# Kernel tuning notes

Measured on AMD Instinct MI355X. Metric: run time of the kernel, lower is better.

Reference implementation:

```python
import jax, jax.numpy as jnp
import numpy as np

C = 64
CQ = C // 8
B, D, H, W = 4, 16, 16, 16


def setup_inputs() -> dict:
    key = jax.random.key(0)
    ks = jax.random.split(key, 8)
    s = 1.0 / np.sqrt(C)
    return {
        "x": jax.random.normal(ks[0], (B, C, D, H, W), jnp.float32),
        "Wq": jax.random.normal(ks[1], (CQ, C), jnp.float32) * s,
        "bq": jax.random.normal(ks[2], (CQ,), jnp.float32) * 0.01,
        "Wk": jax.random.normal(ks[3], (CQ, C), jnp.float32) * s,
        "bk": jax.random.normal(ks[4], (CQ,), jnp.float32) * 0.01,
        "Wv": jax.random.normal(ks[5], (C, C), jnp.float32) * s,
        "bv": jax.random.normal(ks[6], (C,), jnp.float32) * 0.01,
        "gamma": jnp.zeros((1,), jnp.float32) + 0.5,
    }


def reference(x, Wq, bq, Wk, bk, Wv, bv, gamma):
    b, c, d, h, w = x.shape
    n = d * h * w
    xf = x.reshape(b, c, n)  # [b, c, n]
    # 1x1x1 Conv3d == pointwise linear over channel dim
    q = jnp.einsum('oc,bcn->bon', Wq, xf) + bq[None, :, None]  # [b, cq, n]
    k = jnp.einsum('oc,bcn->bon', Wk, xf) + bk[None, :, None]  # [b, cq, n]
    v = jnp.einsum('oc,bcn->bon', Wv, xf) + bv[None, :, None]  # [b, c, n]
    # attn[b, i, j] = softmax_j(q[:, :, i] . k[:, :, j])
    scores = jnp.einsum('bci,bcj->bij', q, k)  # [b, n, n]
    attn = jax.nn.softmax(scores, axis=-1)
    # out = v @ attn^T : out[b, c, i] = sum_j v[b, c, j] * attn[b, i, j]
    out = jnp.einsum('bcj,bij->bci', v, attn).reshape(b, c, d, h, w)
    return gamma * out + x
```

## Files before the change

### kernel.cpp

```cpp
#include <hip/hip_runtime.h>
#include <hip/hip_bf16.h>
#include <cmath>

#define NTOK 4096

typedef float        f32x16 __attribute__((ext_vector_type(16)));
typedef short        s16x8  __attribute__((ext_vector_type(8)));
typedef unsigned int u32x4  __attribute__((ext_vector_type(4)));

__device__ __forceinline__ unsigned short f2bf(float f) {
    __hip_bfloat16 h = __float2bfloat16(f);
    return *reinterpret_cast<unsigned short*>(&h);
}
__device__ __forceinline__ float bf2f(unsigned short u) {
    __hip_bfloat16 h = *reinterpret_cast<__hip_bfloat16*>(&u);
    return __bfloat162float(h);
}
__device__ __forceinline__ unsigned pk2(float a, float b) {
    __hip_bfloat162 h = __float22bfloat162_rn(make_float2(a, b));
    return *reinterpret_cast<unsigned*>(&h);
}

__global__ __launch_bounds__(512)
void qkv_kernel(const float* __restrict__ x,
                const float* __restrict__ Wq, const float* __restrict__ bq,
                const float* __restrict__ Wk, const float* __restrict__ bk,
                const float* __restrict__ Wv, const float* __restrict__ bv,
                unsigned short* __restrict__ qt2, unsigned short* __restrict__ kt2,
                unsigned short* __restrict__ vt)
{
    __shared__ float wlds[80 * 64];
    __shared__ float blds[80];
    __shared__ float pacc[2][4][32][9];

    const int t  = threadIdx.x;
    const int l  = t & 63;
    const int wv = t >> 6;
    const int cq = wv & 3;
    const int cp = wv >> 2;
    const int v  = l & 31;
    const int hh = l >> 5;

    for (int idx = t; idx < 1280; idx += 512) {
        const int row  = idx >> 4;
        const int col4 = idx & 15;
        const float* src = (row < 8)  ? (Wq + row * 64)
                         : (row < 16) ? (Wk + (row - 8) * 64)
                                      : (Wv + (row - 16) * 64);
        ((float4*)wlds)[idx] = ((const float4*)src)[col4];
    }
    if (t < 80)
        blds[t] = (t < 8) ? bq[t] : (t < 16) ? bk[t - 8] : bv[t - 16];
    __syncthreads();

    const int vg = blockIdx.x;
    const int b  = vg >> 7;
    const int i  = ((vg & 127) << 5) + v;

    const float* xb = x + ((size_t)b * 64 + 16 * cq) * NTOK + i;
    float xv[16];
    #pragma unroll
    for (int c = 0; c < 16; c++) xv[c] = xb[(size_t)c * NTOK];

    const size_t row = (size_t)b * NTOK + i;
    const int jl   = i & 15;
    const int slot = (jl & 3) | ((jl & 4) << 1) | ((jl & 8) >> 1);

    #pragma unroll
    for (int s = 0; s < 5; ++s) {
        const int chunk = cp + 2 * s;

        float a[4];
        #pragma unroll
        for (int k = 0; k < 4; k++) a[k] = 0.f;
        #pragma unroll
        for (int c4 = 0; c4 < 4; c4++) {
            #pragma unroll
            for (int k = 0; k < 4; k++) {
                const float4 w4v =
                    ((const float4*)wlds)[(chunk * 8 + 4 * hh + k) * 16 + cq * 4 + c4];
                a[k] += w4v.x * xv[c4*4+0] + w4v.y * xv[c4*4+1]
                      + w4v.z * xv[c4*4+2] + w4v.w * xv[c4*4+3];
            }
        }
        if (s) __syncthreads();
        #pragma unroll
        for (int k = 0; k < 4; k++) pacc[cp][cq][v][4 * hh + k] = a[k];
        __syncthreads();

        const int o = 2 * cq + hh;
        float fin = ((pacc[cp][0][v][o] + pacc[cp][1][v][o])
                  +  (pacc[cp][2][v][o] + pacc[cp][3][v][o]))
                  + blds[chunk * 8 + o];

        if (chunk < 2) {
            if (chunk == 0) fin *= 1.4426950408889634f;
            const unsigned short hu = f2bf(fin);
            const unsigned short lu = f2bf(fin - bf2f(hu));
            unsigned short* dst = (chunk == 0 ? qt2 : kt2) + row * 16;
            dst[o]     = hu;
            dst[8 + o] = lu;
        } else {
            const int c = (chunk - 2) * 8 + o;
            vt[((size_t)b * 256 + (i >> 4)) * 1024 + (size_t)c * 16 + slot] = f2bf(fin);
        }
    }
}

__global__ __launch_bounds__(1024)
void attn_kernel(const unsigned short* __restrict__ qt2,
                 const unsigned short* __restrict__ kt2,
                 const unsigned short* __restrict__ vt,
                 const float* __restrict__ x,
                 const float* __restrict__ gamma,
                 float* __restrict__ out)
{
    __shared__ float slds[4][64][64];
    __shared__ float sldl[4][64];

    const int t    = threadIdx.x;
    const int l    = t & 63;
    const int wv   = t >> 6;
    const int qt   = wv & 1;
    const int u    = wv >> 1;
    const int lo31 = l & 31;
    const int h    = l >> 5;
    const int w     = blockIdx.x;
    const int b     = w >> 6;
    const int qbase = (w & 63) << 6;
    const int j0    = u << 9;

    const unsigned short* qrow =
        qt2 + ((size_t)b * NTOK + qbase + qt * 32 + lo31) * 16;
    s16x8 qB1 = *(const s16x8*)qrow;
    s16x8 qB2;
    if (h == 0) qB2 = *(const s16x8*)(qrow + 8);
    else        { u32x4 z = {0,0,0,0}; qB2 = __builtin_bit_cast(s16x8, z); }

    const unsigned short* kb  = kt2 + (size_t)b * NTOK * 16 + (size_t)h * 8;
    const unsigned short* vbA = vt + (size_t)b * NTOK * 64 + (size_t)lo31 * 16 + 8 * h;
    const unsigned short* vbB = vbA + 512;

    f32x16 accA, accB;
    #pragma unroll
    for (int r = 0; r < 16; r++) { accA[r] = 0.f; accB[r] = 0.f; }
    float lsum = 0.f;

    s16x8 K[2], V00[2], V01[2], V10[2], V11[2];

    #define LOADSET(s_, a_) do {                                              \
        K[s_]   = *(const s16x8*)(kb + (size_t)(j0 + ((a_) << 5) + lo31) * 16);  \
        V00[s_] = *(const s16x8*)(vbA + (size_t)((j0 >> 4) + ((a_) << 1)) * 1024);     \
        V01[s_] = *(const s16x8*)(vbA + (size_t)((j0 >> 4) + ((a_) << 1) + 1) * 1024); \
        V10[s_] = *(const s16x8*)(vbB + (size_t)((j0 >> 4) + ((a_) << 1)) * 1024);     \
        V11[s_] = *(const s16x8*)(vbB + (size_t)((j0 >> 4) + ((a_) << 1) + 1) * 1024); \
    } while (0)

    LOADSET(0, 0);

    #pragma unroll
    for (int it = 0; it < 16; ++it) {
        const int cu = it & 1;
        const int nx = it + 1;
        LOADSET(cu ^ 1, (nx < 16) ? nx : 0);

        f32x16 s;
        #pragma unroll
        for (int r = 0; r < 16; r++) s[r] = 0.f;
        s = __builtin_amdgcn_mfma_f32_32x32x16_bf16(K[cu], qB1, s, 0, 0, 0);
        s = __builtin_amdgcn_mfma_f32_32x32x16_bf16(K[cu], qB2, s, 0, 0, 0);

        #pragma unroll
        for (int r = 0; r < 16; r++) s[r] = __builtin_amdgcn_exp2f(s[r]);

        lsum += ((s[0]+s[1])+(s[2]+s[3])) + ((s[4]+s[5])+(s[6]+s[7]))
              + ((s[8]+s[9])+(s[10]+s[11])) + ((s[12]+s[13])+(s[14]+s[15]));

        u32x4 wa, wc;
        wa.x = pk2(s[0], s[1]);   wa.y = pk2(s[2], s[3]);
        wa.z = pk2(s[4], s[5]);   wa.w = pk2(s[6], s[7]);
        wc.x = pk2(s[8], s[9]);   wc.y = pk2(s[10], s[11]);
        wc.z = pk2(s[12], s[13]); wc.w = pk2(s[14], s[15]);
        s16x8 pf0 = __builtin_bit_cast(s16x8, wa);
        s16x8 pf1 = __builtin_bit_cast(s16x8, wc);

        __builtin_amdgcn_s_setprio(1);
        accA = __builtin_amdgcn_mfma_f32_32x32x16_bf16(V00[cu], pf0, accA, 0, 0, 0);
        accA = __builtin_amdgcn_mfma_f32_32x32x16_bf16(V01[cu], pf1, accA, 0, 0, 0);
        accB = __builtin_amdgcn_mfma_f32_32x32x16_bf16(V10[cu], pf0, accB, 0, 0, 0);
        accB = __builtin_amdgcn_mfma_f32_32x32x16_bf16(V11[cu], pf1, accB, 0, 0, 0);
        __builtin_amdgcn_s_setprio(0);
    }

    lsum += __shfl_xor(lsum, 32);

    #define WR_SLOT(sidx) do {                                                \
        const int s_ = (sidx);                                                \
        _Pragma("unroll")                                                     \
        for (int r = 0; r < 16; r++) {                                        \
            const int c_ = (r & 3) + 8 * (r >> 2) + 4 * h;                    \
            slds[s_][c_][qt * 32 + lo31]      = accA[r];                      \
            slds[s_][c_ + 32][qt * 32 + lo31] = accB[r];                      \
        }                                                                     \
        if (h == 0) sldl[s_][qt * 32 + lo31] = lsum;                          \
    } while (0)

    #define MRG_SLOT(sidx) do {                                               \
        const int s_ = (sidx);                                                \
        _Pragma("unroll")                                                     \
        for (int r = 0; r < 16; r++) {                                        \
            const int c_ = (r & 3) + 8 * (r >> 2) + 4 * h;                    \
            accA[r] += slds[s_][c_][qt * 32 + lo31];                          \
            accB[r] += slds[s_][c_ + 32][qt * 32 + lo31];                     \
        }                                                                     \
        lsum += sldl[s_][qt * 32 + lo31];                                     \
    } while (0)

    if (u >= 4) WR_SLOT(u - 4);
    __syncthreads();
    if (u < 4) MRG_SLOT(u);
    __syncthreads();
    if (u == 2 || u == 3) WR_SLOT(u - 2);
    __syncthreads();
    if (u < 2) MRG_SLOT(u);
    __syncthreads();
    if (u == 1) WR_SLOT(0);
    __syncthreads();
    if (u == 0) { MRG_SLOT(0); WR_SLOT(0); }
    __syncthreads();

    const int c  = t >> 4;
    const int q4 = (t & 15) << 2;
    const float g = gamma[0];
    const float4 a4 = *(const float4*)&slds[0][c][q4];
    const float g0 = g / sldl[0][q4 + 0];
    const float g1 = g / sldl[0][q4 + 1];
    const float g2 = g / sldl[0][q4 + 2];
    const float g3 = g / sldl[0][q4 + 3];
    const size_t off = (((size_t)b * 64 + c) << 12) + qbase + q4;
    const float4 xv4 = *(const float4*)(x + off);
    float4 o;
    o.x = a4.x * g0 + xv4.x;
    o.y = a4.y * g1 + xv4.y;
    o.z = a4.z * g2 + xv4.z;
    o.w = a4.w * g3 + xv4.w;
    *(float4*)(out + off) = o;
}

extern "C" void kernel_launch(void* const* d_in, const int* in_sizes, int n_in,
                              void* d_out, int out_size, void* d_ws, size_t ws_size,
                              hipStream_t stream) {
    const float* x     = (const float*)d_in[0];
    const float* Wq    = (const float*)d_in[1];
    const float* bq    = (const float*)d_in[2];
    const float* Wk    = (const float*)d_in[3];
    const float* bk    = (const float*)d_in[4];
    const float* Wv    = (const float*)d_in[5];
    const float* bv    = (const float*)d_in[6];
    const float* gamma = (const float*)d_in[7];
    float* out = (float*)d_out;

    unsigned short* qt2 = (unsigned short*)d_ws;
    unsigned short* kt2 = qt2 + (size_t)4 * NTOK * 16;
    unsigned short* vt  = kt2 + (size_t)4 * NTOK * 16;

    qkv_kernel<<<512, 512, 0, stream>>>(x, Wq, bq, Wk, bk, Wv, bv, qt2, kt2, vt);
    attn_kernel<<<256, 1024, 0, stream>>>(qt2, kt2, vt, x, gamma, out);
}
```

Measured before the change: 33.82 us.

## Compute QKV projection with bf16 MFMA instead of scalar FMA and LDS reduction

The QKV projection kernel is rewritten to use 32x32x16 bf16 MFMA instructions. Each wave now computes all 80 output rows for 32 tokens directly from global memory, so the LDS weight staging, the cross-wave partial-sum reduction and the barriers are gone. The launch shrinks from 512 blocks of 512 threads to 128 blocks of 256. This rounds x and the weights to bf16 before accumulation, where they were fp32 before, which may hurt accuracy, particularly for the q/k hi-lo split.

```diff
diff --git a/kernel.cpp b/kernel.cpp
--- a/kernel.cpp
+++ b/kernel.cpp
@@ -21,7 +21,7 @@
     return *reinterpret_cast<unsigned*>(&h);
 }
 
-__global__ __launch_bounds__(512)
+__global__ __launch_bounds__(256, 4)
 void qkv_kernel(const float* __restrict__ x,
                 const float* __restrict__ Wq, const float* __restrict__ bq,
                 const float* __restrict__ Wk, const float* __restrict__ bk,
@@ -29,80 +29,85 @@
                 unsigned short* __restrict__ qt2, unsigned short* __restrict__ kt2,
                 unsigned short* __restrict__ vt)
 {
-    __shared__ float wlds[80 * 64];
-    __shared__ float blds[80];
-    __shared__ float pacc[2][4][32][9];
-
-    const int t  = threadIdx.x;
-    const int l  = t & 63;
-    const int wv = t >> 6;
-    const int cq = wv & 3;
-    const int cp = wv >> 2;
-    const int v  = l & 31;
-    const int hh = l >> 5;
-
-    for (int idx = t; idx < 1280; idx += 512) {
-        const int row  = idx >> 4;
-        const int col4 = idx & 15;
-        const float* src = (row < 8)  ? (Wq + row * 64)
-                         : (row < 16) ? (Wk + (row - 8) * 64)
-                                      : (Wv + (row - 16) * 64);
-        ((float4*)wlds)[idx] = ((const float4*)src)[col4];
+    const int t    = threadIdx.x;
+    const int l    = t & 63;
+    const int wv   = t >> 6;
+    const int lo31 = l & 31;
+    const int h    = l >> 5;
+    const int blk  = blockIdx.x;
+    const int b    = blk >> 5;
+    const int i    = ((blk & 31) << 7) + (wv << 5) + lo31;
+
+    const float* xb = x + ((size_t)b * 64) * NTOK + i;
+    s16x8 B0, B1, B2, B3;
+    #define MAKE_B(Bv, ks) do {                                               \
+        const float* src = xb + (size_t)((ks) * 16 + 8 * h) * NTOK;           \
+        float f0 = src[0];                  float f1 = src[NTOK];             \
+        float f2 = src[2 * (size_t)NTOK];   float f3 = src[3 * (size_t)NTOK]; \
+        float f4 = src[4 * (size_t)NTOK];   float f5 = src[5 * (size_t)NTOK]; \
+        float f6 = src[6 * (size_t)NTOK];   float f7 = src[7 * (size_t)NTOK]; \
+        u32x4 p;                                                              \
+        p.x = pk2(f0, f1); p.y = pk2(f2, f3);                                 \
+        p.z = pk2(f4, f5); p.w = pk2(f6, f7);                                 \
+        Bv = __builtin_bit_cast(s16x8, p);                                    \
+    } while (0)
+    MAKE_B(B0, 0); MAKE_B(B1, 1); MAKE_B(B2, 2); MAKE_B(B3, 3);
+
+    f32x16 C0, C1, C2;
+    #pragma unroll
+    for (int r = 0; r < 16; r++) { C0[r] = 0.f; C1[r] = 0.f; C2[r] = 0.f; }
+
+    #pragma unroll
+    for (int tile = 0; tile < 3; tile++) {
+        const int row = tile * 32 + lo31;
+        const bool act = (row < 80);
+        const float* wrow = (row < 8)  ? (Wq + row * 64)
+                          : (row < 16) ? (Wk + (row - 8) * 64)
+                          : act        ? (Wv + (row - 16) * 64)
+                                       : Wq;
+        #pragma unroll
+        for (int ks = 0; ks < 4; ks++) {
+            u32x4 p;
+            if (act) {
+                const float4 f0 = ((const float4*)(wrow + ks * 16 + 8 * h))[0];
+                const float4 f1 = ((const float4*)(wrow + ks * 16 + 8 * h))[1];
+                p.x = pk2(f0.x, f0.y); p.y = pk2(f0.z, f0.w);
+                p.z = pk2(f1.x, f1.y); p.w = pk2(f1.z, f1.w);
+            } else { p.x = 0; p.y = 0; p.z = 0; p.w = 0; }
+            const s16x8 A = __builtin_bit_cast(s16x8, p);
+            const s16x8 Bk = (ks == 0) ? B0 : (ks == 1) ? B1 : (ks == 2) ? B2 : B3;
+            if (tile == 0)      C0 = __builtin_amdgcn_mfma_f32_32x32x16_bf16(A, Bk, C0, 0, 0, 0);
+            else if (tile == 1) C1 = __builtin_amdgcn_mfma_f32_32x32x16_bf16(A, Bk, C1, 0, 0, 0);
+            else                C2 = __builtin_amdgcn_mfma_f32_32x32x16_bf16(A, Bk, C2, 0, 0, 0);
+        }
     }
-    if (t < 80)
-        blds[t] = (t < 8) ? bq[t] : (t < 16) ? bk[t - 8] : bv[t - 16];
-    __syncthreads();
-
-    const int vg = blockIdx.x;
-    const int b  = vg >> 7;
-    const int i  = ((vg & 127) << 5) + v;
-
-    const float* xb = x + ((size_t)b * 64 + 16 * cq) * NTOK + i;
-    float xv[16];
-    #pragma unroll
-    for (int c = 0; c < 16; c++) xv[c] = xb[(size_t)c * NTOK];
-
-    const size_t row = (size_t)b * NTOK + i;
+
+    const size_t rowq = ((size_t)b * NTOK + i) * 16;
     const int jl   = i & 15;
     const int slot = (jl & 3) | ((jl & 4) << 1) | ((jl & 8) >> 1);
-
-    #pragma unroll
-    for (int s = 0; s < 5; ++s) {
-        const int chunk = cp + 2 * s;
-
-        float a[4];
-        #pragma unroll
-        for (int k = 0; k < 4; k++) a[k] = 0.f;
-        #pragma unroll
-        for (int c4 = 0; c4 < 4; c4++) {
-            #pragma unroll
-            for (int k = 0; k < 4; k++) {
-                const float4 w4v =
-                    ((const float4*)wlds)[(chunk * 8 + 4 * hh + k) * 16 + cq * 4 + c4];
-                a[k] += w4v.x * xv[c4*4+0] + w4v.y * xv[c4*4+1]
-                      + w4v.z * xv[c4*4+2] + w4v.w * xv[c4*4+3];
+    const size_t vbase = ((size_t)b * 256 + (i >> 4)) * 1024 + slot;
+
+    #pragma unroll
+    for (int tile = 0; tile < 3; tile++) {
+        #pragma unroll
+        for (int r = 0; r < 16; r++) {
+            const int grow = tile * 32 + (r & 3) + 8 * (r >> 2) + 4 * h;
+            const float cval = (tile == 0) ? C0[r] : (tile == 1) ? C1[r] : C2[r];
+            if (grow < 8) {
+                const float fin = (cval + bq[grow]) * 1.4426950408889634f;
+                const unsigned short hu = f2bf(fin);
+                qt2[rowq + grow]     = hu;
+                qt2[rowq + 8 + grow] = f2bf(fin - bf2f(hu));
+            } else if (grow < 16) {
+                const int o = grow - 8;
+                const float fin = cval + bk[o];
+                const unsigned short hu = f2bf(fin);
+                kt2[rowq + o]     = hu;
+                kt2[rowq + 8 + o] = f2bf(fin - bf2f(hu));
+            } else if (grow < 80) {
+                const int c = grow - 16;
+                vt[vbase + (size_t)c * 16] = f2bf(cval + bv[c]);
             }
-        }
-        if (s) __syncthreads();
-        #pragma unroll
-        for (int k = 0; k < 4; k++) pacc[cp][cq][v][4 * hh + k] = a[k];
-        __syncthreads();
-
-        const int o = 2 * cq + hh;
-        float fin = ((pacc[cp][0][v][o] + pacc[cp][1][v][o])
-                  +  (pacc[cp][2][v][o] + pacc[cp][3][v][o]))
-                  + blds[chunk * 8 + o];
-
-        if (chunk < 2) {
-            if (chunk == 0) fin *= 1.4426950408889634f;
-            const unsigned short hu = f2bf(fin);
-            const unsigned short lu = f2bf(fin - bf2f(hu));
-            unsigned short* dst = (chunk == 0 ? qt2 : kt2) + row * 16;
-            dst[o]     = hu;
-            dst[8 + o] = lu;
-        } else {
-            const int c = (chunk - 2) * 8 + o;
-            vt[((size_t)b * 256 + (i >> 4)) * 1024 + (size_t)c * 16 + slot] = f2bf(fin);
         }
     }
 }
@@ -264,6 +269,6 @@
     unsigned short* kt2 = qt2 + (size_t)4 * NTOK * 16;
     unsigned short* vt  = kt2 + (size_t)4 * NTOK * 16;
 
-    qkv_kernel<<<512, 512, 0, stream>>>(x, Wq, bq, Wk, bk, Wv, bv, qt2, kt2, vt);
+    qkv_kernel<<<128, 256, 0, stream>>>(x, Wq, bq, Wk, bk, Wv, bv, qt2, kt2, vt);
     attn_kernel<<<256, 1024, 0, stream>>>(qt2, kt2, vt, x, gamma, out);
 }
```

Result: faster. 31.31 us, median of 2 (-7.4%).
